# Kernel optimization log

Hardware: AMD Instinct MI355X
Metric: run time of the kernel (lower is better)

The kernel has to match this reference:

```python
import jax, jax.numpy as jnp
import numpy as np

C = 256          # in_channels = out_channels per head
H = 4            # heads
NEG_SLOPE = 0.2  # GATConv leaky_relu slope
EPS = 1e-5       # LayerNorm eps
NUM_LAYERS = 2

# fixed 4-node graph: 9 explicit edges + 4 self loops (PyG GATConv default add_self_loops=True)
SRC = jnp.array([1, 1, 2, 2, 3, 3, 1, 2, 3, 0, 1, 2, 3])
DST = jnp.array([2, 3, 1, 3, 1, 2, 0, 0, 0, 0, 1, 2, 3])
ONEHOT = (DST[:, None] == jnp.arange(4)[None, :]).astype(jnp.float32)  # [E=13, N=4]
MASK = ONEHOT.astype(bool)


def gat_layer(x, W, a_src, a_dst, b):
    """PyG GATConv(C, C, heads=4, concat=False), eval mode (no dropout).
    x: [B,4,C]; W: [C, H*C]; a_src/a_dst: [H,C]; b: [C]."""
    B = x.shape[0]
    xp = (x @ W).reshape(B, 4, H, C)                       # [B,4,H,C]
    e_src = jnp.sum(xp * a_src[None, None], axis=-1)       # [B,4,H]
    e_dst = jnp.sum(xp * a_dst[None, None], axis=-1)       # [B,4,H]
    e = jax.nn.leaky_relu(e_src[:, SRC] + e_dst[:, DST], NEG_SLOPE)  # [B,E,H]
    # softmax over incoming edges per destination node (segment softmax, fixed topology)
    m = jnp.max(jnp.where(MASK[None, :, :, None], e[:, :, None, :], -jnp.inf), axis=1)  # [B,4,H]
    ex = jnp.exp(e - m[:, DST])                            # [B,E,H]
    denom = jnp.einsum('beh,ed->bdh', ex, ONEHOT)          # [B,4,H]
    alpha = ex / denom[:, DST]                             # [B,E,H]
    msg = alpha[..., None] * xp[:, SRC]                    # [B,E,H,C]
    out = jnp.einsum('behc,ed->bdhc', msg, ONEHOT)         # [B,4,H,C]
    return out.mean(axis=2) + b                            # concat=False -> head mean, + bias


def layer_norm(x, g, beta):
    mu = jnp.mean(x, axis=-1, keepdims=True)
    var = jnp.mean((x - mu) ** 2, axis=-1, keepdims=True)
    return (x - mu) * jax.lax.rsqrt(var + EPS) * g + beta


def setup_inputs() -> dict:
    key = jax.random.key(0)
    ks = jax.random.split(key, 20)
    B, HW = 32, 64
    inp = {
        'x_ful': jax.random.normal(ks[0], (B, C, HW, HW), jnp.float32),
        'rgb':   jax.random.normal(ks[1], (B, C, HW, HW), jnp.float32),
        'dep':   jax.random.normal(ks[2], (B, C, HW, HW), jnp.float32),
        'tok':   jax.random.normal(ks[3], (1, C), jnp.float32),
    }
    s = 1.0 / np.sqrt(C)
    for i in range(NUM_LAYERS):
        k = jax.random.split(ks[4 + i], 4)
        inp[f'W{i}'] = jax.random.normal(k[0], (C, H * C), jnp.float32) * s
        inp[f'asrc{i}'] = jax.random.normal(k[1], (H, C), jnp.float32) * s
        inp[f'adst{i}'] = jax.random.normal(k[2], (H, C), jnp.float32) * s
        inp[f'b{i}'] = jnp.zeros((C,), jnp.float32)
        inp[f'g{i}'] = jnp.ones((C,), jnp.float32)
        inp[f'beta{i}'] = jnp.zeros((C,), jnp.float32)
    return inp


def reference(x_ful, rgb, dep, tok,
              W0, asrc0, adst0, b0, g0, beta0,
              W1, asrc1, adst1, b1, g1, beta1):
    B = x_ful.shape[0]
    x1 = rgb.mean(axis=(2, 3))    # squeeze_rgb: global avg pool -> [B,C]
    x2 = dep.mean(axis=(2, 3))
    fu = x_ful.mean(axis=(2, 3))
    tokb = jnp.broadcast_to(tok, (B, C))
    nodes = jnp.stack([tokb, fu, x1, x2], axis=1)  # [B,4,C]

    params = [(W0, asrc0, adst0, b0, g0, beta0), (W1, asrc1, adst1, b1, g1, beta1)]
    g = nodes
    for (W, a_s, a_d, b, gam, bet) in params:
        g = gat_layer(g, W, a_s, a_d, b) + g   # residual
        g = layer_norm(g, gam, bet)
        g = jax.nn.relu(g)

    att = jax.nn.sigmoid(g[:, 0, :])[:, :, None, None]  # token node gates channels
    return x_ful * att + x_ful
```

## Files before the change

### kernel.cpp

```cpp
#include <hip/hip_runtime.h>
#include <hip/hip_bf16.h>

#define CCH 256
#define HEADS 4

typedef float f4 __attribute__((ext_vector_type(4)));

__global__ __launch_bounds__(256) void poolA_kernel(
    const float* __restrict__ rgb, const float* __restrict__ dep,
    float* __restrict__ nodes )
{
    const int rw   = blockIdx.x * 4 + (threadIdx.x >> 6);
    const int lane = threadIdx.x & 63;
    const int tensor = rw >> 13;
    const int row    = rw & 8191;
    const f4* src = (const f4*)((tensor ? dep : rgb) + (size_t)row * 4096);

    f4 v[8];
    f4 acc = {0.f, 0.f, 0.f, 0.f};
#pragma unroll
    for (int j = 0; j < 8; ++j) v[j] = __builtin_nontemporal_load(src + lane + 64 * j);
#pragma unroll
    for (int j = 0; j < 8; ++j) acc += v[j];
#pragma unroll
    for (int j = 0; j < 8; ++j) v[j] = __builtin_nontemporal_load(src + lane + 64 * (8 + j));
#pragma unroll
    for (int j = 0; j < 8; ++j) acc += v[j];

    float s = acc.x + acc.y + acc.z + acc.w;
#pragma unroll
    for (int off = 32; off; off >>= 1) s += __shfl_down(s, off, 64);
    if (lane == 0) {
        const int b = row >> 8, c = row & 255;
        nodes[(size_t)b * 1024 + (2 + tensor) * CCH + c] = s * (1.f / 4096.f);
    }
}

__global__ __launch_bounds__(256) void poolB_kernel(
    const float* __restrict__ xf, float* __restrict__ nodes)
{
    const int row  = blockIdx.x * 4 + (threadIdx.x >> 6);
    const int lane = threadIdx.x & 63;
    const f4* src = (const f4*)(xf + (size_t)row * 4096);

    f4 v[8];
    f4 acc = {0.f, 0.f, 0.f, 0.f};
#pragma unroll
    for (int j = 0; j < 8; ++j) v[j] = src[lane + 64 * j];
#pragma unroll
    for (int j = 0; j < 8; ++j) acc += v[j];
#pragma unroll
    for (int j = 0; j < 8; ++j) v[j] = src[lane + 64 * (8 + j)];
#pragma unroll
    for (int j = 0; j < 8; ++j) acc += v[j];

    float s = acc.x + acc.y + acc.z + acc.w;
#pragma unroll
    for (int off = 32; off; off >>= 1) s += __shfl_down(s, off, 64);
    if (lane == 0) {
        const int b = row >> 8, c = row & 255;
        nodes[(size_t)b * 1024 + 1 * CCH + c] = s * (1.f / 4096.f);
    }
}

__global__ __launch_bounds__(256) void gat_kernel(
    const float* __restrict__ nodes, const float* __restrict__ tok,
    float* __restrict__ scale,
    const float* __restrict__ W0, const float* __restrict__ as0,
    const float* __restrict__ ad0, const float* __restrict__ b0,
    const float* __restrict__ g0, const float* __restrict__ be0,
    const float* __restrict__ W1, const float* __restrict__ as1,
    const float* __restrict__ ad1, const float* __restrict__ b1,
    const float* __restrict__ g1, const float* __restrict__ be1)
{
    const int t = threadIdx.x;
    const int b = blockIdx.x;
    const int lane = t & 63, wv = t >> 6;

    __shared__ float gl[4][CCH];
    __shared__ float redl[4][32];
    __shared__ float esed[32];
    __shared__ float alpha_s[4][4][4];
    __shared__ float red2[4][8];
    __shared__ float mu_s[4], rstd_s[4];

    gl[0][t] = tok[t];
    gl[1][t] = nodes[(size_t)b * 1024 + 256 + t];
    gl[2][t] = nodes[(size_t)b * 1024 + 512 + t];
    gl[3][t] = nodes[(size_t)b * 1024 + 768 + t];
    __syncthreads();

    for (int layer = 0; layer < 2; ++layer) {
        const float* W  = layer ? W1  : W0;
        const float* As = layer ? as1 : as0;
        const float* Ad = layer ? ad1 : ad0;
        const float* Bi = layer ? b1  : b0;
        const float* Ga = layer ? g1  : g0;
        const float* Be = layer ? be1 : be0;

        float acc[4][4];
#pragma unroll
        for (int j = 0; j < 4; ++j)
#pragma unroll
            for (int n = 0; n < 4; ++n) acc[j][n] = 0.f;

        const float* Wp = W + t;
        for (int k0 = 0; k0 < 256; k0 += 8) {
            float wr[8][4];
#pragma unroll
            for (int u = 0; u < 8; ++u)
#pragma unroll
                for (int j = 0; j < 4; ++j)
                    wr[u][j] = Wp[(k0 + u) * 1024 + j * 256];
#pragma unroll
            for (int u = 0; u < 8; ++u) {
                float g0v = gl[0][k0 + u], g1v = gl[1][k0 + u];
                float g2v = gl[2][k0 + u], g3v = gl[3][k0 + u];
#pragma unroll
                for (int j = 0; j < 4; ++j) {
                    float w = wr[u][j];
                    acc[j][0] += g0v * w;
                    acc[j][1] += g1v * w;
                    acc[j][2] += g2v * w;
                    acc[j][3] += g3v * w;
                }
            }
        }

        float asr[4], adr[4];
#pragma unroll
        for (int j = 0; j < 4; ++j) { asr[j] = As[j * 256 + t]; adr[j] = Ad[j * 256 + t]; }
        float rv[32];
#pragma unroll
        for (int n = 0; n < 4; ++n)
#pragma unroll
            for (int j = 0; j < 4; ++j) {
                rv[n * 4 + j]      = acc[j][n] * asr[j];
                rv[16 + n * 4 + j] = acc[j][n] * adr[j];
            }
#pragma unroll
        for (int i = 0; i < 32; ++i)
#pragma unroll
            for (int off = 32; off; off >>= 1)
                rv[i] += __shfl_down(rv[i], off, 64);
        if (lane == 0) {
#pragma unroll
            for (int i = 0; i < 32; ++i) redl[wv][i] = rv[i];
        }
        __syncthreads();
        if (t < 32) esed[t] = redl[0][t] + redl[1][t] + redl[2][t] + redl[3][t];
        __syncthreads();

        if (t < 16) {
            const int d = t >> 2, hh = t & 3;
            const int cnt[4]     = {4, 3, 3, 3};
            const int srcs[4][4] = {{1,2,3,0},{2,3,1,0},{1,3,2,0},{1,2,3,0}};
            float v[4];
            float m = -1e30f;
            const int n = cnt[d];
            for (int s = 0; s < n; ++s) {
                float e = esed[srcs[d][s] * 4 + hh] + esed[16 + d * 4 + hh];
                e = (e >= 0.f) ? e : 0.2f * e;
                v[s] = e; m = fmaxf(m, e);
            }
            float den = 0.f;
            for (int s = 0; s < n; ++s) { v[s] = expf(v[s] - m); den += v[s]; }
            float inv = 1.f / den;
            for (int s = 0; s < n; ++s) alpha_s[d][hh][s] = v[s] * inv;
            for (int s = n; s < 4; ++s) alpha_s[d][hh][s] = 0.f;
        }
        __syncthreads();

        const int srcs2[4][4] = {{1,2,3,0},{2,3,1,0},{1,3,2,0},{1,2,3,0}};
        float bi = Bi[t];
        float gv[4];
#pragma unroll
        for (int d = 0; d < 4; ++d) {
            float sum = 0.f;
#pragma unroll
            for (int j = 0; j < 4; ++j) {
                float mj = 0.f;
#pragma unroll
                for (int s = 0; s < 4; ++s)
                    mj += alpha_s[d][j][s] * acc[j][srcs2[d][s]];
                sum += mj;
            }
            gv[d] = 0.25f * sum + bi + gl[d][t];
        }

        float rv2[8];
#pragma unroll
        for (int d = 0; d < 4; ++d) { rv2[d * 2] = gv[d]; rv2[d * 2 + 1] = gv[d] * gv[d]; }
#pragma unroll
        for (int i = 0; i < 8; ++i)
#pragma unroll
            for (int off = 32; off; off >>= 1)
                rv2[i] += __shfl_down(rv2[i], off, 64);
        if (lane == 0) {
#pragma unroll
            for (int i = 0; i < 8; ++i) red2[wv][i] = rv2[i];
        }
        __syncthreads();
        if (t < 4) {
            float s = red2[0][t*2]   + red2[1][t*2]   + red2[2][t*2]   + red2[3][t*2];
            float q = red2[0][t*2+1] + red2[1][t*2+1] + red2[2][t*2+1] + red2[3][t*2+1];
            float mu  = s * (1.f / 256.f);
            float var = q * (1.f / 256.f) - mu * mu;
            mu_s[t]   = mu;
            rstd_s[t] = rsqrtf(var + 1e-5f);
        }
        __syncthreads();
        float ga = Ga[t], be = Be[t];
#pragma unroll
        for (int d = 0; d < 4; ++d) {
            float y = (gv[d] - mu_s[d]) * rstd_s[d] * ga + be;
            gl[d][t] = fmaxf(y, 0.f);
        }
        __syncthreads();
    }

    float x = gl[0][t];
    scale[(size_t)b * CCH + t] = 1.f + 1.f / (1.f + expf(-x));
}

__global__ __launch_bounds__(256) void apply_kernel(
    const float* __restrict__ xf, const float* __restrict__ scale,
    float* __restrict__ out, int total4)
{
    int idx = blockIdx.x * 256 + threadIdx.x;
    const int stride = gridDim.x * 256;
    const f4* in4 = (const f4*)xf;
    f4* out4 = (f4*)out;
    for (; idx < total4; idx += stride) {
        f4 v = in4[idx];
        const float s = scale[idx >> 10];
        f4 o = v * s;
        __builtin_nontemporal_store(o, out4 + idx);
    }
}

extern "C" void kernel_launch(void* const* d_in, const int* in_sizes, int n_in,
                              void* d_out, int out_size, void* d_ws, size_t ws_size,
                              hipStream_t stream) {
    const float* x_ful = (const float*)d_in[0];
    const float* rgb   = (const float*)d_in[1];
    const float* dep   = (const float*)d_in[2];
    const float* tok   = (const float*)d_in[3];
    const float* W0  = (const float*)d_in[4];
    const float* as0 = (const float*)d_in[5];
    const float* ad0 = (const float*)d_in[6];
    const float* b0  = (const float*)d_in[7];
    const float* g0  = (const float*)d_in[8];
    const float* be0 = (const float*)d_in[9];
    const float* W1  = (const float*)d_in[10];
    const float* as1 = (const float*)d_in[11];
    const float* ad1 = (const float*)d_in[12];
    const float* b1  = (const float*)d_in[13];
    const float* g1  = (const float*)d_in[14];
    const float* be1 = (const float*)d_in[15];

    float* nodes = (float*)d_ws;
    float* scale = (float*)((char*)d_ws + 32 * 4 * CCH * sizeof(float));
    float* out   = (float*)d_out;

    poolA_kernel<<<4096, 256, 0, stream>>>(rgb, dep, nodes);
    poolB_kernel<<<2048, 256, 0, stream>>>(x_ful, nodes);
    gat_kernel<<<32, 256, 0, stream>>>(nodes, tok, scale,
                                       W0, as0, ad0, b0, g0, be0,
                                       W1, as1, ad1, b1, g1, be1);
    const int total4 = 32 * CCH * 64 * 64 / 4;
    apply_kernel<<<2048, 256, 0, stream>>>(x_ful, scale, out, total4);
}
```

Before: 154.3 us.

## Merge pooling kernels and split GAT matmul K-dimension across two thread halves

Fuses the two global-average-pool kernels into one 6144-block launch covering rgb, dep and x_ful, keeping nontemporal loads for rgb/dep and cached loads for x_ful. The GAT kernel doubles its block to 512 threads so each half computes half of the K=256 reduction, combining partial sums through shared memory before the attention and layernorm steps. This removes one launch and the tail between pooling kernels, and halves the serial weight-read loop in the tiny 32-block GAT kernel. The cost is extra shared memory, an added barrier, and idle upper-half threads during the epilogue.

```diff
diff --git a/kernel.cpp b/kernel.cpp
--- a/kernel.cpp
+++ b/kernel.cpp
@@ -6,64 +6,51 @@
 
 typedef float f4 __attribute__((ext_vector_type(4)));
 
-__global__ __launch_bounds__(256) void poolA_kernel(
+__global__ __launch_bounds__(256) void pool_kernel(
     const float* __restrict__ rgb, const float* __restrict__ dep,
-    float* __restrict__ nodes )
+    const float* __restrict__ xf, float* __restrict__ nodes )
 {
     const int rw   = blockIdx.x * 4 + (threadIdx.x >> 6);
     const int lane = threadIdx.x & 63;
     const int tensor = rw >> 13;
     const int row    = rw & 8191;
-    const f4* src = (const f4*)((tensor ? dep : rgb) + (size_t)row * 4096);
-
-    f4 v[8];
+    const float* base = (tensor == 0) ? rgb : (tensor == 1) ? dep : xf;
+    const f4* src = (const f4*)(base + (size_t)row * 4096);
+
     f4 acc = {0.f, 0.f, 0.f, 0.f};
-#pragma unroll
-    for (int j = 0; j < 8; ++j) v[j] = __builtin_nontemporal_load(src + lane + 64 * j);
-#pragma unroll
-    for (int j = 0; j < 8; ++j) acc += v[j];
-#pragma unroll
-    for (int j = 0; j < 8; ++j) v[j] = __builtin_nontemporal_load(src + lane + 64 * (8 + j));
-#pragma unroll
-    for (int j = 0; j < 8; ++j) acc += v[j];
+    if (tensor < 2) {
+        f4 v[8];
+#pragma unroll
+        for (int j = 0; j < 8; ++j) v[j] = __builtin_nontemporal_load(src + lane + 64 * j);
+#pragma unroll
+        for (int j = 0; j < 8; ++j) acc += v[j];
+#pragma unroll
+        for (int j = 0; j < 8; ++j) v[j] = __builtin_nontemporal_load(src + lane + 64 * (8 + j));
+#pragma unroll
+        for (int j = 0; j < 8; ++j) acc += v[j];
+    } else {
+        f4 v[8];
+#pragma unroll
+        for (int j = 0; j < 8; ++j) v[j] = src[lane + 64 * j];
+#pragma unroll
+        for (int j = 0; j < 8; ++j) acc += v[j];
+#pragma unroll
+        for (int j = 0; j < 8; ++j) v[j] = src[lane + 64 * (8 + j)];
+#pragma unroll
+        for (int j = 0; j < 8; ++j) acc += v[j];
+    }
 
     float s = acc.x + acc.y + acc.z + acc.w;
 #pragma unroll
     for (int off = 32; off; off >>= 1) s += __shfl_down(s, off, 64);
     if (lane == 0) {
         const int b = row >> 8, c = row & 255;
-        nodes[(size_t)b * 1024 + (2 + tensor) * CCH + c] = s * (1.f / 4096.f);
-    }
-}
-
-__global__ __launch_bounds__(256) void poolB_kernel(
-    const float* __restrict__ xf, float* __restrict__ nodes)
-{
-    const int row  = blockIdx.x * 4 + (threadIdx.x >> 6);
-    const int lane = threadIdx.x & 63;
-    const f4* src = (const f4*)(xf + (size_t)row * 4096);
-
-    f4 v[8];
-    f4 acc = {0.f, 0.f, 0.f, 0.f};
-#pragma unroll
-    for (int j = 0; j < 8; ++j) v[j] = src[lane + 64 * j];
-#pragma unroll
-    for (int j = 0; j < 8; ++j) acc += v[j];
-#pragma unroll
-    for (int j = 0; j < 8; ++j) v[j] = src[lane + 64 * (8 + j)];
-#pragma unroll
-    for (int j = 0; j < 8; ++j) acc += v[j];
-
-    float s = acc.x + acc.y + acc.z + acc.w;
-#pragma unroll
-    for (int off = 32; off; off >>= 1) s += __shfl_down(s, off, 64);
-    if (lane == 0) {
-        const int b = row >> 8, c = row & 255;
-        nodes[(size_t)b * 1024 + 1 * CCH + c] = s * (1.f / 4096.f);
-    }
-}
-
-__global__ __launch_bounds__(256) void gat_kernel(
+        const int nrow = (tensor == 2) ? 1 : (2 + tensor);
+        nodes[(size_t)b * 1024 + nrow * CCH + c] = s * (1.f / 4096.f);
+    }
+}
+
+__global__ __launch_bounds__(512) void gat_kernel(
     const float* __restrict__ nodes, const float* __restrict__ tok,
     float* __restrict__ scale,
     const float* __restrict__ W0, const float* __restrict__ as0,
@@ -75,19 +62,23 @@
 {
     const int t = threadIdx.x;
     const int b = blockIdx.x;
+    const int c = t & 255, kh = t >> 8;
     const int lane = t & 63, wv = t >> 6;
 
     __shared__ float gl[4][CCH];
+    __shared__ float xpart[4][4][CCH];
     __shared__ float redl[4][32];
     __shared__ float esed[32];
     __shared__ float alpha_s[4][4][4];
     __shared__ float red2[4][8];
     __shared__ float mu_s[4], rstd_s[4];
 
-    gl[0][t] = tok[t];
-    gl[1][t] = nodes[(size_t)b * 1024 + 256 + t];
-    gl[2][t] = nodes[(size_t)b * 1024 + 512 + t];
-    gl[3][t] = nodes[(size_t)b * 1024 + 768 + t];
+    if (t < 256) {
+        gl[0][c] = tok[c];
+        gl[1][c] = nodes[(size_t)b * 1024 + 256 + c];
+        gl[2][c] = nodes[(size_t)b * 1024 + 512 + c];
+        gl[3][c] = nodes[(size_t)b * 1024 + 768 + c];
+    }
     __syncthreads();
 
     for (int layer = 0; layer < 2; ++layer) {
@@ -104,18 +95,20 @@
 #pragma unroll
             for (int n = 0; n < 4; ++n) acc[j][n] = 0.f;
 
-        const float* Wp = W + t;
-        for (int k0 = 0; k0 < 256; k0 += 8) {
+        const float* Wp = W + c;
+        const int kbase = kh * 128;
+        for (int k0 = 0; k0 < 128; k0 += 8) {
             float wr[8][4];
 #pragma unroll
             for (int u = 0; u < 8; ++u)
 #pragma unroll
                 for (int j = 0; j < 4; ++j)
-                    wr[u][j] = Wp[(k0 + u) * 1024 + j * 256];
+                    wr[u][j] = Wp[(size_t)(kbase + k0 + u) * 1024 + j * 256];
 #pragma unroll
             for (int u = 0; u < 8; ++u) {
-                float g0v = gl[0][k0 + u], g1v = gl[1][k0 + u];
-                float g2v = gl[2][k0 + u], g3v = gl[3][k0 + u];
+                const int k = kbase + k0 + u;
+                float g0v = gl[0][k], g1v = gl[1][k];
+                float g2v = gl[2][k], g3v = gl[3][k];
 #pragma unroll
                 for (int j = 0; j < 4; ++j) {
                     float w = wr[u][j];
@@ -126,26 +119,41 @@
                 }
             }
         }
-
-        float asr[4], adr[4];
-#pragma unroll
-        for (int j = 0; j < 4; ++j) { asr[j] = As[j * 256 + t]; adr[j] = Ad[j * 256 + t]; }
-        float rv[32];
-#pragma unroll
-        for (int n = 0; n < 4; ++n)
-#pragma unroll
-            for (int j = 0; j < 4; ++j) {
-                rv[n * 4 + j]      = acc[j][n] * asr[j];
-                rv[16 + n * 4 + j] = acc[j][n] * adr[j];
-            }
-#pragma unroll
-        for (int i = 0; i < 32; ++i)
-#pragma unroll
-            for (int off = 32; off; off >>= 1)
-                rv[i] += __shfl_down(rv[i], off, 64);
-        if (lane == 0) {
-#pragma unroll
-            for (int i = 0; i < 32; ++i) redl[wv][i] = rv[i];
+        if (kh == 1) {
+#pragma unroll
+            for (int j = 0; j < 4; ++j)
+#pragma unroll
+                for (int n = 0; n < 4; ++n) xpart[j][n][c] = acc[j][n];
+        }
+        __syncthreads();
+
+        float gv[4];
+        if (kh == 0) {
+#pragma unroll
+            for (int j = 0; j < 4; ++j)
+#pragma unroll
+                for (int n = 0; n < 4; ++n) acc[j][n] += xpart[j][n][c];
+
+            float asr[4], adr[4];
+#pragma unroll
+            for (int j = 0; j < 4; ++j) { asr[j] = As[j * 256 + c]; adr[j] = Ad[j * 256 + c]; }
+            float rv[32];
+#pragma unroll
+            for (int n = 0; n < 4; ++n)
+#pragma unroll
+                for (int j = 0; j < 4; ++j) {
+                    rv[n * 4 + j]      = acc[j][n] * asr[j];
+                    rv[16 + n * 4 + j] = acc[j][n] * adr[j];
+                }
+#pragma unroll
+            for (int i = 0; i < 32; ++i)
+#pragma unroll
+                for (int off = 32; off; off >>= 1)
+                    rv[i] += __shfl_down(rv[i], off, 64);
+            if (lane == 0) {
+#pragma unroll
+                for (int i = 0; i < 32; ++i) redl[wv][i] = rv[i];
+            }
         }
         __syncthreads();
         if (t < 32) esed[t] = redl[0][t] + redl[1][t] + redl[2][t] + redl[3][t];
@@ -171,34 +179,35 @@
         }
         __syncthreads();
 
-        const int srcs2[4][4] = {{1,2,3,0},{2,3,1,0},{1,3,2,0},{1,2,3,0}};
-        float bi = Bi[t];
-        float gv[4];
-#pragma unroll
-        for (int d = 0; d < 4; ++d) {
-            float sum = 0.f;
-#pragma unroll
-            for (int j = 0; j < 4; ++j) {
-                float mj = 0.f;
-#pragma unroll
-                for (int s = 0; s < 4; ++s)
-                    mj += alpha_s[d][j][s] * acc[j][srcs2[d][s]];
-                sum += mj;
-            }
-            gv[d] = 0.25f * sum + bi + gl[d][t];
-        }
-
-        float rv2[8];
-#pragma unroll
-        for (int d = 0; d < 4; ++d) { rv2[d * 2] = gv[d]; rv2[d * 2 + 1] = gv[d] * gv[d]; }
-#pragma unroll
-        for (int i = 0; i < 8; ++i)
-#pragma unroll
-            for (int off = 32; off; off >>= 1)
-                rv2[i] += __shfl_down(rv2[i], off, 64);
-        if (lane == 0) {
-#pragma unroll
-            for (int i = 0; i < 8; ++i) red2[wv][i] = rv2[i];
+        if (kh == 0) {
+            const int srcs2[4][4] = {{1,2,3,0},{2,3,1,0},{1,3,2,0},{1,2,3,0}};
+            float bi = Bi[c];
+#pragma unroll
+            for (int d = 0; d < 4; ++d) {
+                float sum = 0.f;
+#pragma unroll
+                for (int j = 0; j < 4; ++j) {
+                    float mj = 0.f;
+#pragma unroll
+                    for (int s = 0; s < 4; ++s)
+                        mj += alpha_s[d][j][s] * acc[j][srcs2[d][s]];
+                    sum += mj;
+                }
+                gv[d] = 0.25f * sum + bi + gl[d][c];
+            }
+
+            float rv2[8];
+#pragma unroll
+            for (int d = 0; d < 4; ++d) { rv2[d * 2] = gv[d]; rv2[d * 2 + 1] = gv[d] * gv[d]; }
+#pragma unroll
+            for (int i = 0; i < 8; ++i)
+#pragma unroll
+                for (int off = 32; off; off >>= 1)
+                    rv2[i] += __shfl_down(rv2[i], off, 64);
+            if (lane == 0) {
+#pragma unroll
+                for (int i = 0; i < 8; ++i) red2[wv][i] = rv2[i];
+            }
         }
         __syncthreads();
         if (t < 4) {
@@ -210,17 +219,21 @@
             rstd_s[t] = rsqrtf(var + 1e-5f);
         }
         __syncthreads();
-        float ga = Ga[t], be = Be[t];
-#pragma unroll
-        for (int d = 0; d < 4; ++d) {
-            float y = (gv[d] - mu_s[d]) * rstd_s[d] * ga + be;
-            gl[d][t] = fmaxf(y, 0.f);
-        }
-        __syncthreads();
-    }
-
-    float x = gl[0][t];
-    scale[(size_t)b * CCH + t] = 1.f + 1.f / (1.f + expf(-x));
+        if (kh == 0) {
+            float ga = Ga[c], be = Be[c];
+#pragma unroll
+            for (int d = 0; d < 4; ++d) {
+                float y = (gv[d] - mu_s[d]) * rstd_s[d] * ga + be;
+                gl[d][c] = fmaxf(y, 0.f);
+            }
+        }
+        __syncthreads();
+    }
+
+    if (t < 256) {
+        float x = gl[0][c];
+        scale[(size_t)b * CCH + c] = 1.f + 1.f / (1.f + expf(-x));
+    }
 }
 
 __global__ __launch_bounds__(256) void apply_kernel(
@@ -263,9 +276,8 @@
     float* scale = (float*)((char*)d_ws + 32 * 4 * CCH * sizeof(float));
     float* out   = (float*)d_out;
 
-    poolA_kernel<<<4096, 256, 0, stream>>>(rgb, dep, nodes);
-    poolB_kernel<<<2048, 256, 0, stream>>>(x_ful, nodes);
-    gat_kernel<<<32, 256, 0, stream>>>(nodes, tok, scale,
+    pool_kernel<<<6144, 256, 0, stream>>>(rgb, dep, x_ful, nodes);
+    gat_kernel<<<32, 512, 0, stream>>>(nodes, tok, scale,
                                        W0, as0, ad0, b0, g0, be0,
                                        W1, as1, ad1, b1, g1, be1);
     const int total4 = 32 * CCH * 64 * 64 / 4;
```

Result: slower. 196.9 us (+27.6%).
